# Performance work log

Measured on AMD Instinct MI355X. Metric: run time of the kernel, lower is better.

The kernel has to match this reference:

```python
import jax, jax.numpy as jnp
import numpy as np

B, T, D = 4, 2048, 1024
H = 16
HD = D // H  # 64

def setup_inputs() -> dict:
    key = jax.random.key(0)
    ks = jax.random.split(key, 7)
    s = 1.0 / np.sqrt(D)
    x = jax.random.normal(ks[0], (B, T, D), dtype=jnp.float32)
    # Per-head query projections stacked: Wq[h] maps D -> HD
    Wq = jax.random.uniform(ks[1], (H, D, HD), minval=-s, maxval=s, dtype=jnp.float32)
    bq = jax.random.uniform(ks[2], (H, HD), minval=-s, maxval=s, dtype=jnp.float32)
    Wk = jax.random.uniform(ks[3], (D, HD), minval=-s, maxval=s, dtype=jnp.float32)
    bk = jax.random.uniform(ks[4], (HD,), minval=-s, maxval=s, dtype=jnp.float32)
    Wv = jax.random.uniform(ks[5], (D, HD), minval=-s, maxval=s, dtype=jnp.float32)
    bv = jax.random.uniform(ks[6], (HD,), minval=-s, maxval=s, dtype=jnp.float32)
    return {"x": x, "Wq": Wq, "bq": bq, "Wk": Wk, "bk": bk, "Wv": Wv, "bv": bv}

def reference(x, Wq, bq, Wk, bk, Wv, bv):
    # shared single K/V head: [B, T, HD]
    k = jnp.einsum('btd,de->bte', x, Wk) + bk
    v = jnp.einsum('btd,de->bte', x, Wv) + bv
    # per-head queries batched: [B, H, T, HD]
    q = jnp.einsum('btd,hde->bhte', x, Wq) + bq[:, None, :]
    scale = 1.0 / jnp.sqrt(jnp.asarray(HD, dtype=x.dtype))
    scores = jnp.einsum('bhqe,bke->bhqk', q, k) * scale  # [B, H, T, T]
    attn = jax.nn.softmax(scores, axis=-1)
    out = jnp.einsum('bhqk,bke->bhqe', attn, v)  # [B, H, T, HD]
    # concat heads along last dim (head order matches torch cat order)
    return jnp.transpose(out, (0, 2, 1, 3)).reshape(B, T, H * HD)
```

## Files before the change

kernel.cpp:

```cpp
#include <hip/hip_runtime.h>

#define B 4
#define T 2048
#define D 1024
#define H 16
#define HD 64
#define NKT 32

typedef __attribute__((ext_vector_type(8))) short bf16x8;
typedef __attribute__((ext_vector_type(4))) float f32x4;
typedef __attribute__((ext_vector_type(16))) float f32x16;

#define MFMA16(a, b, c) __builtin_amdgcn_mfma_f32_16x16x32_bf16(a, b, c, 0, 0, 0)
#define MFMA32(a, b, c) __builtin_amdgcn_mfma_f32_32x32x16_bf16(a, b, c, 0, 0, 0)

static __device__ __forceinline__ unsigned short f2bf(float f) {
    union { float f; unsigned u; } v; v.f = f;
    unsigned r = v.u + 0x7FFFu + ((v.u >> 16) & 1u);
    return (unsigned short)(r >> 16);
}

static __device__ __forceinline__ bf16x8 cvt8(const float* p) {
    float4 a = *(const float4*)p;
    float4 b = *(const float4*)(p + 4);
    bf16x8 r;
    r[0] = (short)f2bf(a.x); r[1] = (short)f2bf(a.y);
    r[2] = (short)f2bf(a.z); r[3] = (short)f2bf(a.w);
    r[4] = (short)f2bf(b.x); r[5] = (short)f2bf(b.y);
    r[6] = (short)f2bf(b.z); r[7] = (short)f2bf(b.w);
    return r;
}

static __device__ __forceinline__ unsigned cvtpk(float lo, float hi) {
    unsigned r;
    asm("v_cvt_pk_bf16_f32 %0, %1, %2" : "=v"(r) : "v"(lo), "v"(hi));
    return r;
}

static __device__ __forceinline__ float fmax3(float a, float b, float c) {
    return fmaxf(fmaxf(a, b), c);
}

static __device__ __forceinline__ f32x16 zero16() {
    f32x16 z;
#pragma unroll
    for (int i = 0; i < 16; ++i) z[i] = 0.f;
    return z;
}

static __device__ __forceinline__ float xhalf_max(float x) {
    unsigned u = __float_as_uint(x);
    auto r = __builtin_amdgcn_permlane32_swap(u, u, false, false);
    return fmaxf(__uint_as_float(r[0]), __uint_as_float(r[1]));
}
static __device__ __forceinline__ float xhalf_sum(float x) {
    unsigned u = __float_as_uint(x);
    auto r = __builtin_amdgcn_permlane32_swap(u, u, false, false);
    return __uint_as_float(r[0]) + __uint_as_float(r[1]);
}

typedef __attribute__((address_space(1))) const unsigned char gl_u8;
typedef __attribute__((address_space(3))) unsigned char lds_u8;

static __device__ __forceinline__ void stage16(const void* g, void* l) {
    __builtin_amdgcn_global_load_lds((gl_u8*)(unsigned long long)g,
                                     (lds_u8*)(unsigned int)(unsigned long long)l,
                                     16, 0, 0);
}

__global__ __launch_bounds__(256) void pack_w(const float* __restrict__ Wq,
                                              const float* __restrict__ Wk,
                                              const float* __restrict__ Wv,
                                              unsigned short* __restrict__ Wqt,
                                              unsigned short* __restrict__ Wkt,
                                              unsigned short* __restrict__ Wvt) {
    __shared__ float tile[64][65];
    int hh = blockIdx.x >> 4, db = blockIdx.x & 15;
    const float* src;
    unsigned short* dst;
    if (hh < 16)      { src = Wq + (size_t)hh * D * HD; dst = Wqt + (size_t)hh * HD * D; }
    else if (hh == 16){ src = Wk; dst = Wkt; }
    else              { src = Wv; dst = Wvt; }
    int r = threadIdx.x >> 6, c = threadIdx.x & 63;
    int d0 = db * 64;
#pragma unroll
    for (int i = 0; i < 16; ++i)
        tile[r * 16 + i][c] = src[(size_t)(d0 + r * 16 + i) * HD + c];
    __syncthreads();
#pragma unroll
    for (int j = 0; j < 16; ++j)
        dst[(size_t)(r * 16 + j) * D + d0 + c] = f2bf(tile[c][r * 16 + j]);
}

__global__ __launch_bounds__(256) void kv_gemm(const float* __restrict__ xf,
                                               const unsigned short* __restrict__ Wkt,
                                               const unsigned short* __restrict__ Wvt,
                                               const float* __restrict__ bk,
                                               const float* __restrict__ bv,
                                               unsigned short* __restrict__ xbf,
                                               unsigned char* __restrict__ Ksw,
                                               unsigned char* __restrict__ Vsw) {
    int rt  = blockIdx.x * 2 + (threadIdx.x >> 7);
    int grp = (threadIdx.x >> 6) & 1;
    int lane = threadIdx.x & 63;
    int ln = lane & 15, lk = lane >> 4;
    int t0 = rt * 16;

    const unsigned short* Wt = grp ? Wvt : Wkt;
    const float* bias = grp ? bv : bk;

    f32x4 acc[4];
#pragma unroll
    for (int e = 0; e < 4; ++e) acc[e] = (f32x4){0.f, 0.f, 0.f, 0.f};

    for (int d0 = 0; d0 < D; d0 += 32) {
        size_t xi = (size_t)(t0 + ln) * D + d0 + lk * 8;
        bf16x8 a = cvt8(xf + xi);
        if (grp == 0) *(bf16x8*)(xbf + xi) = a;
#pragma unroll
        for (int e = 0; e < 4; ++e) {
            bf16x8 w = *(const bf16x8*)(Wt + (size_t)(e * 16 + ln) * D + d0 + lk * 8);
            acc[e] = MFMA16(a, w, acc[e]);
        }
    }

#pragma unroll
    for (int e = 0; e < 4; ++e)
#pragma unroll
        for (int r = 0; r < 4; ++r) {
            int trow = t0 + lk * 4 + r;
            float val = acc[e][r] + bias[e * 16 + ln];
            int bb = trow >> 11, tl = trow & 2047;
            size_t tbase = ((size_t)(bb * NKT + (tl >> 6))) << 13;
            int key = tl & 63;
            if (grp == 0) {
                int off = (e * 2 + (key >> 5)) * 1024 +
                          ((ln >> 3) * 32 + (key & 31)) * 16 + (ln & 7) * 2;
                *(unsigned short*)(Ksw + tbase + off) = f2bf(val);
            } else {
                int off = ((key >> 4) * 2 + (e >> 1)) * 1024 +
                          (((key >> 3) & 1) * 32 + (e & 1) * 16 + ln) * 16 +
                          (key & 7) * 2;
                *(unsigned short*)(Vsw + tbase + off) = f2bf(val);
            }
        }
}

__global__ __launch_bounds__(256, 4) void attn(const unsigned short* __restrict__ xbf,
                                               const unsigned short* __restrict__ Wqt,
                                               const float* __restrict__ bq,
                                               const unsigned char* __restrict__ Ksw,
                                               const unsigned char* __restrict__ Vsw,
                                               float* __restrict__ out) {
    __shared__ __align__(16) unsigned char smem[32768];

    int blk = ((blockIdx.x & 7) << 7) | (blockIdx.x >> 3);
    int qt = blk & 15;
    int h  = (blk >> 4) & 15;
    int b  = blk >> 8;
    int wave = threadIdx.x >> 6, lane = threadIdx.x & 63;
    int l31 = lane & 31, hi = lane >> 5;
    int t0 = qt * 128 + wave * 32;

    const unsigned char* Kt = Ksw + (((size_t)b * NKT) << 13);
    const unsigned char* Vt = Vsw + (((size_t)b * NKT) << 13);
    int soff = wave * 1024 + lane * 16;
    int ldsw = wave * 1024;

    auto STAGE = [&](int kt, int lk, int lv) {
        const unsigned char* gK = Kt + ((size_t)kt << 13);
        const unsigned char* gV = Vt + ((size_t)kt << 13);
        stage16(gK + soff,        smem + lk + ldsw);
        stage16(gK + 4096 + soff, smem + lk + 4096 + ldsw);
        stage16(gV + soff,        smem + lv + ldsw);
        stage16(gV + 4096 + soff, smem + lv + 4096 + ldsw);
    };

    STAGE(0, 0, 16384);

    f32x16 qacc[2] = {zero16(), zero16()};
    const unsigned short* Wh = Wqt + (size_t)h * HD * D;
    const unsigned short* xrow  = xbf + (size_t)(b * T + t0 + l31) * D + hi * 8;
    const unsigned short* wrow0 = Wh + (size_t)l31 * D + hi * 8;
    const unsigned short* wrow1 = Wh + (size_t)(32 + l31) * D + hi * 8;
    for (int dk = 0; dk < D; dk += 16) {
        bf16x8 xb = *(const bf16x8*)(xrow + dk);
        qacc[0] = MFMA32(*(const bf16x8*)(wrow0 + dk), xb, qacc[0]);
        qacc[1] = MFMA32(*(const bf16x8*)(wrow1 + dk), xb, qacc[1]);
    }

    const float sl2 = 0.125f * 1.44269504f;
    float qv[2][16];
#pragma unroll
    for (int e0 = 0; e0 < 2; ++e0)
#pragma unroll
        for (int r = 0; r < 16; ++r) {
            int crow = (r & 3) + 8 * (r >> 2) + 4 * hi;
            qv[e0][r] = (qacc[e0][r] + bq[h * HD + e0 * 32 + crow]) * sl2;
        }

    bf16x8 qf[4];
#pragma unroll
    for (int dt = 0; dt < 4; ++dt) {
        int s = dt >> 1;
        int b0 = 8 * (dt & 1), b1 = b0 + 4;
        unsigned c0 = cvtpk(qv[s][b0 + 0], qv[s][b0 + 1]);
        unsigned c1 = cvtpk(qv[s][b0 + 2], qv[s][b0 + 3]);
        unsigned c2 = cvtpk(qv[s][b1 + 0], qv[s][b1 + 1]);
        unsigned c3 = cvtpk(qv[s][b1 + 2], qv[s][b1 + 3]);
        auto r02 = __builtin_amdgcn_permlane32_swap(c0, c2, false, false);
        auto r13 = __builtin_amdgcn_permlane32_swap(c1, c3, false, false);
        union { unsigned u[4]; bf16x8 v; } pu;
        pu.u[0] = r02[0]; pu.u[1] = r13[0]; pu.u[2] = r02[1]; pu.u[3] = r13[1];
        qf[dt] = pu.v;
    }

    const unsigned char* fbase = smem + lane * 16;

    __syncthreads();

    float mrun = -1e30f, lrun = 0.f;
    f32x16 o[2] = {zero16(), zero16()};

    auto PHASE = [&](int ck, int cv, int ph) {
        f32x16 s = zero16();
#pragma unroll
        for (int dt = 0; dt < 4; ++dt) {
            bf16x8 kf = *(const bf16x8*)(fbase + ck + (dt * 2 + ph) * 1024);
            s = MFMA32(kf, qf[dt], s);
        }

        float m0 = fmax3(s[0], s[1], s[2]);
        float m1 = fmax3(s[3], s[4], s[5]);
        float m2 = fmax3(s[6], s[7], s[8]);
        float m3 = fmax3(s[9], s[10], s[11]);
        float m4 = fmax3(s[12], s[13], s[14]);
        float y0 = fmax3(m0, m1, m2);
        float y1 = fmax3(m3, m4, s[15]);
        float pmax = xhalf_max(fmaxf(y0, y1));

        if (__any(pmax - mrun > 8.0f)) {
            float newm = fmaxf(mrun, pmax);
            float corr = __builtin_amdgcn_exp2f(mrun - newm);
            mrun = newm;
            lrun *= corr;
#pragma unroll
            for (int e0 = 0; e0 < 2; ++e0)
#pragma unroll
                for (int r = 0; r < 16; ++r) o[e0][r] *= corr;
        }

#pragma unroll
        for (int r = 0; r < 16; ++r)
            s[r] = __builtin_amdgcn_exp2f(s[r] - mrun);

        float sm[8];
#pragma unroll
        for (int i = 0; i < 8; ++i) sm[i] = s[i] + s[i + 8];
#pragma unroll
        for (int i = 0; i < 4; ++i) sm[i] += sm[i + 4];
        float rsum = (sm[0] + sm[1]) + (sm[2] + sm[3]);
        lrun += xhalf_sum(rsum);

#pragma unroll
        for (int ks = 0; ks < 2; ++ks) {
            int b0 = 8 * ks, b1 = b0 + 4;
            bf16x8 vf0 = *(const bf16x8*)(fbase + cv + ((ph * 2 + ks) * 2 + 0) * 1024);
            bf16x8 vf1 = *(const bf16x8*)(fbase + cv + ((ph * 2 + ks) * 2 + 1) * 1024);
            unsigned c0 = cvtpk(s[b0 + 0], s[b0 + 1]);
            unsigned c1 = cvtpk(s[b0 + 2], s[b0 + 3]);
            unsigned c2 = cvtpk(s[b1 + 0], s[b1 + 1]);
            unsigned c3 = cvtpk(s[b1 + 2], s[b1 + 3]);
            auto r02 = __builtin_amdgcn_permlane32_swap(c0, c2, false, false);
            auto r13 = __builtin_amdgcn_permlane32_swap(c1, c3, false, false);
            union { unsigned u[4]; bf16x8 v; } pu;
            pu.u[0] = r02[0]; pu.u[1] = r13[0]; pu.u[2] = r02[1]; pu.u[3] = r13[1];
            o[0] = MFMA32(vf0, pu.v, o[0]);
            o[1] = MFMA32(vf1, pu.v, o[1]);
        }
    };

    auto TILE = [&](int ck, int cv, int nxt, int nk, int nv) {
        if (nxt < NKT) STAGE(nxt, nk, nv);
        PHASE(ck, cv, 0);
        PHASE(ck, cv, 1);
        __syncthreads();
    };

    for (int kt = 0; kt < NKT; kt += 2) {
        TILE(0,    16384, kt + 1, 8192, 24576);
        TILE(8192, 24576, kt + 2, 0,    16384);
    }

    float inv = 1.f / lrun;
    unsigned char* eb = smem + wave * 8192;
#pragma unroll
    for (int e0 = 0; e0 < 2; ++e0)
#pragma unroll
        for (int r = 0; r < 16; ++r) {
            int crow = (r & 3) + 8 * (r >> 2) + 4 * hi;
            int col4 = (e0 * 32 + crow) * 4;
            *(float*)(eb + l31 * 256 + (col4 ^ ((l31 & 15) << 4))) = o[e0][r] * inv;
        }
    __syncthreads();

    int rgrp = lane >> 4;
    int c16 = (lane & 15) * 16;
#pragma unroll
    for (int g = 0; g < 8; ++g) {
        int row = g * 4 + rgrp;
        float4 vv = *(const float4*)(eb + row * 256 + (c16 ^ ((row & 15) << 4)));
        *(float4*)(out + (size_t)(b * T + t0 + row) * D + h * HD + (c16 >> 2)) = vv;
    }
}

extern "C" void kernel_launch(void* const* d_in, const int* in_sizes, int n_in,
                              void* d_out, int out_size, void* d_ws, size_t ws_size,
                              hipStream_t stream) {
    const float* x  = (const float*)d_in[0];
    const float* Wq = (const float*)d_in[1];
    const float* bq = (const float*)d_in[2];
    const float* Wk = (const float*)d_in[3];
    const float* bk = (const float*)d_in[4];
    const float* Wv = (const float*)d_in[5];
    const float* bv = (const float*)d_in[6];
    float* out = (float*)d_out;

    unsigned char* ws = (unsigned char*)d_ws;
    unsigned short* xbf = (unsigned short*)(ws);
    unsigned short* Wqt = (unsigned short*)(ws + 16777216);
    unsigned short* Wkt = (unsigned short*)(ws + 18874368);
    unsigned short* Wvt = (unsigned short*)(ws + 19005440);
    unsigned char*  Ksw = ws + 19136512;
    unsigned char*  Vsw = ws + 20185088;

    pack_w<<<288, 256, 0, stream>>>(Wq, Wk, Wv, Wqt, Wkt, Wvt);
    kv_gemm<<<256, 256, 0, stream>>>(x, Wkt, Wvt, bk, bv, xbf, Ksw, Vsw);
    attn<<<1024, 256, 0, stream>>>(xbf, Wqt, bq, Ksw, Vsw, out);
}
```

Before: 183.0 us.

## Shrink attention blocks to two waves, read V from global, store output directly

Attention blocks drop from four waves to two, each covering 64 query rows, and the launch doubles to 2048 blocks. Only K tiles are now staged in LDS (16KB double buffer). V fragments are loaded straight from global memory, relying on the pre-swizzled layout. The output epilogue writes float4 directly from registers instead of transposing through LDS. This cuts LDS use and a barrier and should allow more resident blocks, but each block now reloads K/V and recomputes its Q projection for fewer rows, and the direct V loads add global latency inside the inner loop.

```diff
diff --git a/kernel.cpp b/kernel.cpp
--- a/kernel.cpp
+++ b/kernel.cpp
@@ -146,37 +146,35 @@
         }
 }
 
-__global__ __launch_bounds__(256, 4) void attn(const unsigned short* __restrict__ xbf,
-                                               const unsigned short* __restrict__ Wqt,
-                                               const float* __restrict__ bq,
-                                               const unsigned char* __restrict__ Ksw,
-                                               const unsigned char* __restrict__ Vsw,
-                                               float* __restrict__ out) {
-    __shared__ __align__(16) unsigned char smem[32768];
-
-    int blk = ((blockIdx.x & 7) << 7) | (blockIdx.x >> 3);
-    int qt = blk & 15;
-    int h  = (blk >> 4) & 15;
-    int b  = blk >> 8;
+__global__ __launch_bounds__(128) void attn(const unsigned short* __restrict__ xbf,
+                                            const unsigned short* __restrict__ Wqt,
+                                            const float* __restrict__ bq,
+                                            const unsigned char* __restrict__ Ksw,
+                                            const unsigned char* __restrict__ Vsw,
+                                            float* __restrict__ out) {
+    __shared__ __align__(16) unsigned char smem[16384];
+
+    int nb = blockIdx.x;
+    int blk = ((nb & 7) << 8) | (nb >> 3);
+    int qt = blk & 31;
+    int h  = (blk >> 5) & 15;
+    int b  = blk >> 9;
     int wave = threadIdx.x >> 6, lane = threadIdx.x & 63;
     int l31 = lane & 31, hi = lane >> 5;
-    int t0 = qt * 128 + wave * 32;
+    int t0 = qt * 64 + wave * 32;
 
     const unsigned char* Kt = Ksw + (((size_t)b * NKT) << 13);
     const unsigned char* Vt = Vsw + (((size_t)b * NKT) << 13);
     int soff = wave * 1024 + lane * 16;
-    int ldsw = wave * 1024;
-
-    auto STAGE = [&](int kt, int lk, int lv) {
-        const unsigned char* gK = Kt + ((size_t)kt << 13);
-        const unsigned char* gV = Vt + ((size_t)kt << 13);
-        stage16(gK + soff,        smem + lk + ldsw);
-        stage16(gK + 4096 + soff, smem + lk + 4096 + ldsw);
-        stage16(gV + soff,        smem + lv + ldsw);
-        stage16(gV + 4096 + soff, smem + lv + 4096 + ldsw);
+
+    auto STAGEK = [&](int kt, int lb) {
+        const unsigned char* g = Kt + ((size_t)kt << 13);
+#pragma unroll
+        for (int i = 0; i < 4; ++i)
+            stage16(g + i * 2048 + soff, smem + lb + i * 2048 + soff);
     };
 
-    STAGE(0, 0, 16384);
+    STAGEK(0, 0);
 
     f32x16 qacc[2] = {zero16(), zero16()};
     const unsigned short* Wh = Wqt + (size_t)h * HD * D;
@@ -216,13 +214,14 @@
     }
 
     const unsigned char* fbase = smem + lane * 16;
+    const unsigned char* vlane = Vt + lane * 16;
 
     __syncthreads();
 
     float mrun = -1e30f, lrun = 0.f;
     f32x16 o[2] = {zero16(), zero16()};
 
-    auto PHASE = [&](int ck, int cv, int ph) {
+    auto PHASE = [&](int ck, const unsigned char* vtile, int ph) {
         f32x16 s = zero16();
 #pragma unroll
         for (int dt = 0; dt < 4; ++dt) {
@@ -265,8 +264,8 @@
 #pragma unroll
         for (int ks = 0; ks < 2; ++ks) {
             int b0 = 8 * ks, b1 = b0 + 4;
-            bf16x8 vf0 = *(const bf16x8*)(fbase + cv + ((ph * 2 + ks) * 2 + 0) * 1024);
-            bf16x8 vf1 = *(const bf16x8*)(fbase + cv + ((ph * 2 + ks) * 2 + 1) * 1024);
+            bf16x8 vf0 = *(const bf16x8*)(vtile + ((ph * 2 + ks) * 2 + 0) * 1024);
+            bf16x8 vf1 = *(const bf16x8*)(vtile + ((ph * 2 + ks) * 2 + 1) * 1024);
             unsigned c0 = cvtpk(s[b0 + 0], s[b0 + 1]);
             unsigned c1 = cvtpk(s[b0 + 2], s[b0 + 3]);
             unsigned c2 = cvtpk(s[b1 + 0], s[b1 + 1]);
@@ -280,38 +279,32 @@
         }
     };
 
-    auto TILE = [&](int ck, int cv, int nxt, int nk, int nv) {
-        if (nxt < NKT) STAGE(nxt, nk, nv);
-        PHASE(ck, cv, 0);
-        PHASE(ck, cv, 1);
+    auto TILE = [&](int ck, int kt, int nxt, int nk) {
+        if (nxt < NKT) STAGEK(nxt, nk);
+        const unsigned char* vtile = vlane + ((size_t)kt << 13);
+        PHASE(ck, vtile, 0);
+        PHASE(ck, vtile, 1);
         __syncthreads();
     };
 
     for (int kt = 0; kt < NKT; kt += 2) {
-        TILE(0,    16384, kt + 1, 8192, 24576);
-        TILE(8192, 24576, kt + 2, 0,    16384);
+        TILE(0,    kt,     kt + 1, 8192);
+        TILE(8192, kt + 1, kt + 2, 0);
     }
 
     float inv = 1.f / lrun;
-    unsigned char* eb = smem + wave * 8192;
+    float* orow = out + (size_t)(b * T + t0 + l31) * D + h * HD + 4 * hi;
 #pragma unroll
     for (int e0 = 0; e0 < 2; ++e0)
 #pragma unroll
-        for (int r = 0; r < 16; ++r) {
-            int crow = (r & 3) + 8 * (r >> 2) + 4 * hi;
-            int col4 = (e0 * 32 + crow) * 4;
-            *(float*)(eb + l31 * 256 + (col4 ^ ((l31 & 15) << 4))) = o[e0][r] * inv;
-        }
-    __syncthreads();
-
-    int rgrp = lane >> 4;
-    int c16 = (lane & 15) * 16;
-#pragma unroll
-    for (int g = 0; g < 8; ++g) {
-        int row = g * 4 + rgrp;
-        float4 vv = *(const float4*)(eb + row * 256 + (c16 ^ ((row & 15) << 4)));
-        *(float4*)(out + (size_t)(b * T + t0 + row) * D + h * HD + (c16 >> 2)) = vv;
-    }
+        for (int g = 0; g < 4; ++g) {
+            float4 vv;
+            vv.x = o[e0][g * 4 + 0] * inv;
+            vv.y = o[e0][g * 4 + 1] * inv;
+            vv.z = o[e0][g * 4 + 2] * inv;
+            vv.w = o[e0][g * 4 + 3] * inv;
+            *(float4*)(orow + e0 * 32 + g * 8) = vv;
+        }
 }
 
 extern "C" void kernel_launch(void* const* d_in, const int* in_sizes, int n_in,
@@ -336,5 +329,5 @@
 
     pack_w<<<288, 256, 0, stream>>>(Wq, Wk, Wv, Wqt, Wkt, Wvt);
     kv_gemm<<<256, 256, 0, stream>>>(x, Wkt, Wvt, bk, bv, xbf, Ksw, Vsw);
-    attn<<<1024, 256, 0, stream>>>(xbf, Wqt, bq, Ksw, Vsw, out);
-}
+    attn<<<2048, 128, 0, stream>>>(xbf, Wqt, bq, Ksw, Vsw, out);
+}
```

Result: slower. 217.5 us (+18.8%).
